# Optimization experiments

Hardware: AMD Instinct MI355X
Metric: run time of the kernel (lower is better)

Reference implementation:

```python
import jax, jax.numpy as jnp
import numpy as np

N_NODES = 100000
N_EDGES = 1600000
D_IN = 64
D_OUT = 64


def setup_inputs() -> dict:
    key = jax.random.key(0)
    k1, k2, k3, k4, k5 = jax.random.split(key, 5)
    features = jax.random.normal(k1, (N_NODES, D_IN), dtype=jnp.float32)
    edge_row = jax.random.randint(k2, (N_EDGES,), 0, N_NODES, dtype=jnp.int32)
    edge_col = jax.random.randint(k3, (N_EDGES,), 0, N_NODES, dtype=jnp.int32)
    edge_val = jax.random.uniform(k4, (N_EDGES,), dtype=jnp.float32)
    # learned parameters (xavier-uniform kernel, zero bias, ones skip weight)
    limit = float(np.sqrt(6.0 / (D_IN + D_OUT)))
    kernel = jax.random.uniform(k5, (D_IN, D_OUT), minval=-limit, maxval=limit, dtype=jnp.float32)
    bias = jnp.zeros((D_OUT,), dtype=jnp.float32)
    skip_weight = jnp.ones((D_OUT,), dtype=jnp.float32)
    return {
        "features": features,
        "kernel": kernel,
        "bias": bias,
        "skip_weight": skip_weight,
        "edge_row": edge_row,
        "edge_col": edge_col,
        "edge_val": edge_val,
    }


def reference(features, kernel, bias, skip_weight, edge_row, edge_col, edge_val):
    # dense projection: [n, d_in] @ [d_in, d_out]
    h = features @ kernel
    # SpMM: (A h)[r] = sum_{edges e with row r} val_e * h[col_e]
    gathered = h[edge_col] * edge_val[:, None]  # [n_edges, d_out]
    agg = jax.ops.segment_sum(gathered, edge_row, num_segments=N_NODES)
    out = h * skip_weight + agg + bias
    return jax.nn.selu(out)
```

## Files before the change

kernel.cpp:

```cpp
#include <hip/hip_runtime.h>
#include <math.h>

#define N_NODES 100000
#define N_EDGES 1600000
#define D 64
#define RPB 128
#define NBUK 782
#define CAP 3072
#define NGB 782
#define NHB 392
#define EPB 4096
#define POFF_STRIDE 392

typedef unsigned int u32;
typedef unsigned short u16;

static __device__ __forceinline__ u32 f2bf(float x) {
    u32 u = __float_as_uint(x);
    u32 r = u + 0x7FFFu + ((u >> 16) & 1u);
    return r >> 16;
}
static __device__ __forceinline__ u32 pack2(float a, float b) {
    return f2bf(a) | (f2bf(b) << 16);
}
static __device__ __forceinline__ float bflo(u32 u) { return __uint_as_float(u << 16); }
static __device__ __forceinline__ float bfhi(u32 u) { return __uint_as_float(u & 0xFFFF0000u); }
static __device__ __forceinline__ float selu(float x) {
    const float scale = 1.0507009873554805f;
    const float alpha = 1.6732632423543772f;
    return x > 0.f ? scale * x : scale * alpha * (expf(x) - 1.f);
}

__global__ __launch_bounds__(256) void fused_gemm_sort(
    const float* __restrict__ feat, const float* __restrict__ kern,
    const int* __restrict__ erow, const int* __restrict__ ecol,
    const float* __restrict__ eval, u16* __restrict__ hbf,
    int2* __restrict__ sedge, u32* __restrict__ poff)
{
    __shared__ u32 smem[4096];
    const int t = threadIdx.x;

    if (blockIdx.x >= NHB) {
        float* ks = (float*)smem;
        {
            const float4* k4 = (const float4*)kern;
            float4* ks4 = (float4*)ks;
            #pragma unroll
            for (int i = 0; i < 4; i++) ks4[t + 256 * i] = k4[t + 256 * i];
        }
        __syncthreads();

        const int cgi  = t & 7;
        const int rg   = t >> 3;
        const int row0 = (blockIdx.x - NHB) * RPB + rg * 4;

        float4 acc[4][2];
        #pragma unroll
        for (int r = 0; r < 4; r++)
            #pragma unroll
            for (int i = 0; i < 2; i++)
                acc[r][i] = make_float4(0.f, 0.f, 0.f, 0.f);

        #pragma unroll 4
        for (int s = 0; s < 16; s++) {
            float4 f[4];
            #pragma unroll
            for (int r = 0; r < 4; r++) {
                int row = min(row0 + r, N_NODES - 1);
                f[r] = ((const float4*)(feat + (size_t)row * D))[s];
            }
            float4 kk[4][2];
            #pragma unroll
            for (int kv = 0; kv < 4; kv++)
                #pragma unroll
                for (int i = 0; i < 2; i++)
                    kk[kv][i] = ((const float4*)(ks + (s * 4 + kv) * D))[cgi * 2 + i];
            #pragma unroll
            for (int r = 0; r < 4; r++) {
                #pragma unroll
                for (int kv = 0; kv < 4; kv++) {
                    float fv = (&f[r].x)[kv];
                    #pragma unroll
                    for (int i = 0; i < 2; i++) {
                        acc[r][i].x += fv * kk[kv][i].x;
                        acc[r][i].y += fv * kk[kv][i].y;
                        acc[r][i].z += fv * kk[kv][i].z;
                        acc[r][i].w += fv * kk[kv][i].w;
                    }
                }
            }
        }

        #pragma unroll
        for (int r = 0; r < 4; r++) {
            int row = row0 + r;
            if (row < N_NODES) {
                uint4 o;
                o.x = pack2(acc[r][0].x, acc[r][0].y);
                o.y = pack2(acc[r][0].z, acc[r][0].w);
                o.z = pack2(acc[r][1].x, acc[r][1].y);
                o.w = pack2(acc[r][1].z, acc[r][1].w);
                ((uint4*)(hbf + (size_t)row * D))[cgi] = o;
            }
        }
    } else {
        u32* c    = smem;
        u32* o    = c + NBUK;
        u32* cu   = o + NBUK + 1;
        u32* part = cu + NBUK;

        for (int i = t; i < NBUK; i += 256) c[i] = 0u;
        __syncthreads();

        const int hb   = blockIdx.x;
        const int base = hb * EPB;

        #pragma unroll
        for (int k = 0; k < 16; k++) {
            int i = base + k * 256 + t;
            if (i < N_EDGES) atomicAdd(&c[(u32)erow[i] >> 7], 1u);
        }
        __syncthreads();

        const int i0 = t * 4;
        {
            u32 p = 0u;
            #pragma unroll
            for (int j = 0; j < 4; j++) { int i = i0 + j; if (i < NBUK) p += c[i]; }
            part[t] = p;
        }
        __syncthreads();
        for (int d = 1; d < 256; d <<= 1) {
            u32 a = (t >= d) ? part[t - d] : 0u;
            __syncthreads();
            part[t] += a;
            __syncthreads();
        }
        {
            u32 run = (t > 0) ? part[t - 1] : 0u;
            #pragma unroll
            for (int j = 0; j < 4; j++) {
                int i = i0 + j;
                if (i < NBUK) { o[i] = run; cu[i] = run; run += c[i]; }
            }
            if (t == 255) o[NBUK] = part[255];
        }
        __syncthreads();

        #pragma unroll
        for (int k = 0; k < 16; k++) {
            int i = base + k * 256 + t;
            if (i < N_EDGES) {
                u32 r = (u32)erow[i];
                u32 rk = atomicAdd(&cu[r >> 7], 1u);
                sedge[(size_t)hb * EPB + rk] =
                    make_int2(ecol[i] | (int)((r & 127u) << 17),
                              __float_as_int(eval[i]));
            }
        }

        for (int i = t; i <= NBUK; i += 256)
            poff[(size_t)i * POFF_STRIDE + hb] = o[i];
    }
}

__global__ __launch_bounds__(1024) void agg_kernel(
    const u32* __restrict__ poff, const int2* __restrict__ sedge,
    const u16* __restrict__ hbf, const float* __restrict__ skip,
    const float* __restrict__ bias, float* __restrict__ out)
{
    __shared__ int2 eB[CAP];
    __shared__ u32 c[RPB];
    __shared__ u32 o[RPB];
    __shared__ u32 cur[RPB];
    __shared__ u32 rs0[NHB];
    __shared__ u32 rlen[NHB];

    const int t = threadIdx.x;
    const int w = t >> 6;
    const int lane = t & 63;
    const int b = blockIdx.x;

    if (t < RPB) c[t] = 0u;
    if (t < NHB) {
        u32 s0 = poff[(size_t)b * POFF_STRIDE + t];
        u32 s1 = poff[(size_t)(b + 1) * POFF_STRIDE + t];
        rs0[t]  = s0;
        rlen[t] = s1 - s0;
    }
    __syncthreads();

    for (int hb = w; hb < NHB; hb += 16) {
        u32 s0 = rs0[hb], len = rlen[hb];
        for (u32 j = (u32)lane; j < len; j += 64u) {
            int x = sedge[(size_t)hb * EPB + s0 + j].x;
            atomicAdd(&c[(u32)x >> 17], 1u);
        }
    }
    __syncthreads();

    if (t < RPB) o[t] = c[t];
    __syncthreads();
    for (int d = 1; d < RPB; d <<= 1) {
        u32 a = 0u;
        if (t < RPB && t >= d) a = o[t - d];
        __syncthreads();
        if (t < RPB) o[t] += a;
        __syncthreads();
    }
    if (t < RPB) { u32 e = o[t] - c[t]; o[t] = e; cur[t] = e; }
    __syncthreads();

    for (int hb = w; hb < NHB; hb += 16) {
        u32 s0 = rs0[hb], len = rlen[hb];
        for (u32 j = (u32)lane; j < len; j += 64u) {
            int2 e = sedge[(size_t)hb * EPB + s0 + j];
            u32 rl = (u32)e.x >> 17;
            u32 rk = atomicAdd(&cur[rl], 1u);
            if (rk < CAP) eB[rk] = make_int2(e.x & 0x1FFFF, e.y);
        }
    }
    __syncthreads();

    const int rows = min(RPB, N_NODES - b * RPB);
    const int g  = t >> 3;
    const int dg = t & 7;

    float a0 = 0.f, a1 = 0.f, a2 = 0.f, a3 = 0.f;
    float a4 = 0.f, a5 = 0.f, a6 = 0.f, a7 = 0.f;

    u32 jb = 0u, jend = 0u;
    if (g < rows) {
        jb = o[g];
        jend = min(jb + c[g], (u32)CAP);
    }

    u32 j = jb;
    for (; j + 3u < jend; j += 4u) {
        int2 e0 = eB[j];
        int2 e1 = eB[j + 1u];
        int2 e2 = eB[j + 2u];
        int2 e3 = eB[j + 3u];
        float v0 = __int_as_float(e0.y);
        float v1 = __int_as_float(e1.y);
        float v2 = __int_as_float(e2.y);
        float v3 = __int_as_float(e3.y);
        uint4 h0 = ((const uint4*)(hbf + (size_t)e0.x * D))[dg];
        uint4 h1 = ((const uint4*)(hbf + (size_t)e1.x * D))[dg];
        uint4 h2 = ((const uint4*)(hbf + (size_t)e2.x * D))[dg];
        uint4 h3 = ((const uint4*)(hbf + (size_t)e3.x * D))[dg];
        a0 += v0 * bflo(h0.x); a1 += v0 * bfhi(h0.x);
        a2 += v0 * bflo(h0.y); a3 += v0 * bfhi(h0.y);
        a4 += v0 * bflo(h0.z); a5 += v0 * bfhi(h0.z);
        a6 += v0 * bflo(h0.w); a7 += v0 * bfhi(h0.w);
        a0 += v1 * bflo(h1.x); a1 += v1 * bfhi(h1.x);
        a2 += v1 * bflo(h1.y); a3 += v1 * bfhi(h1.y);
        a4 += v1 * bflo(h1.z); a5 += v1 * bfhi(h1.z);
        a6 += v1 * bflo(h1.w); a7 += v1 * bfhi(h1.w);
        a0 += v2 * bflo(h2.x); a1 += v2 * bfhi(h2.x);
        a2 += v2 * bflo(h2.y); a3 += v2 * bfhi(h2.y);
        a4 += v2 * bflo(h2.z); a5 += v2 * bfhi(h2.z);
        a6 += v2 * bflo(h2.w); a7 += v2 * bfhi(h2.w);
        a0 += v3 * bflo(h3.x); a1 += v3 * bfhi(h3.x);
        a2 += v3 * bflo(h3.y); a3 += v3 * bfhi(h3.y);
        a4 += v3 * bflo(h3.z); a5 += v3 * bfhi(h3.z);
        a6 += v3 * bflo(h3.w); a7 += v3 * bfhi(h3.w);
    }
    for (; j < jend; j++) {
        int2 e0 = eB[j];
        float v0 = __int_as_float(e0.y);
        uint4 h0 = ((const uint4*)(hbf + (size_t)e0.x * D))[dg];
        a0 += v0 * bflo(h0.x); a1 += v0 * bfhi(h0.x);
        a2 += v0 * bflo(h0.y); a3 += v0 * bfhi(h0.y);
        a4 += v0 * bflo(h0.z); a5 += v0 * bfhi(h0.z);
        a6 += v0 * bflo(h0.w); a7 += v0 * bfhi(h0.w);
    }

    if (g < rows) {
        const int grow = b * RPB + g;
        uint4 hr = ((const uint4*)(hbf + (size_t)grow * D))[dg];
        float4 s0 = ((const float4*)skip)[2 * dg];
        float4 s1 = ((const float4*)skip)[2 * dg + 1];
        float4 b0 = ((const float4*)bias)[2 * dg];
        float4 b1 = ((const float4*)bias)[2 * dg + 1];
        float4 x0, x1;
        x0.x = selu(bflo(hr.x) * s0.x + b0.x + a0);
        x0.y = selu(bfhi(hr.x) * s0.y + b0.y + a1);
        x0.z = selu(bflo(hr.y) * s0.z + b0.z + a2);
        x0.w = selu(bfhi(hr.y) * s0.w + b0.w + a3);
        x1.x = selu(bflo(hr.z) * s1.x + b1.x + a4);
        x1.y = selu(bfhi(hr.z) * s1.y + b1.y + a5);
        x1.z = selu(bflo(hr.w) * s1.z + b1.z + a6);
        x1.w = selu(bfhi(hr.w) * s1.w + b1.w + a7);
        ((float4*)(out + (size_t)grow * D))[2 * dg]     = x0;
        ((float4*)(out + (size_t)grow * D))[2 * dg + 1] = x1;
    }
}

extern "C" void kernel_launch(void* const* d_in, const int* in_sizes, int n_in,
                              void* d_out, int out_size, void* d_ws, size_t ws_size,
                              hipStream_t stream)
{
    const float* feat = (const float*)d_in[0];
    const float* kern = (const float*)d_in[1];
    const float* bias = (const float*)d_in[2];
    const float* skip = (const float*)d_in[3];
    const int*   erow = (const int*)d_in[4];
    const int*   ecol = (const int*)d_in[5];
    const float* eval = (const float*)d_in[6];
    float* out = (float*)d_out;

    u16*  hbf   = (u16*)d_ws;
    u32*  poff  = (u32*)(hbf + (size_t)N_NODES * D);
    int2* sedge = (int2*)(poff + 306936);

    hipLaunchKernelGGL(fused_gemm_sort, dim3(NGB + NHB), dim3(256), 0, stream,
                       feat, kern, erow, ecol, eval, hbf, sedge, poff);
    hipLaunchKernelGGL(agg_kernel, dim3(NBUK), dim3(1024), 0, stream,
                       poff, sedge, hbf, skip, bias, out);
}
```

Before: 195.0 us.

## Flatten per-bucket edge gather with prefix scan and stage edges in LDS

The aggregation kernel used to walk the 392 bucket segments one wavefront at a time, with mostly idle lanes on short segments, and it read each edge from global memory twice. Now it prefix-scans the segment lengths, has all 1024 threads sweep a flattened edge index using a binary search to locate each segment, and caches the edges in a new LDS buffer eA. The second pass then reads from LDS instead of global memory. This costs extra LDS (another CAP int2 array), a 512-wide scan with several barriers, and a per-edge binary search. Edges beyond CAP are now dropped before counting rather than after the atomic rank.

```diff
diff --git a/kernel.cpp b/kernel.cpp
--- a/kernel.cpp
+++ b/kernel.cpp
@@ -169,33 +169,51 @@
     const u16* __restrict__ hbf, const float* __restrict__ skip,
     const float* __restrict__ bias, float* __restrict__ out)
 {
+    __shared__ int2 eA[CAP];
     __shared__ int2 eB[CAP];
     __shared__ u32 c[RPB];
     __shared__ u32 o[RPB];
     __shared__ u32 cur[RPB];
     __shared__ u32 rs0[NHB];
-    __shared__ u32 rlen[NHB];
+    __shared__ u32 rb[NHB + 1];
+    __shared__ u32 scn[512];
 
     const int t = threadIdx.x;
-    const int w = t >> 6;
-    const int lane = t & 63;
     const int b = blockIdx.x;
 
     if (t < RPB) c[t] = 0u;
+    u32 mylen = 0u;
     if (t < NHB) {
         u32 s0 = poff[(size_t)b * POFF_STRIDE + t];
         u32 s1 = poff[(size_t)(b + 1) * POFF_STRIDE + t];
-        rs0[t]  = s0;
-        rlen[t] = s1 - s0;
-    }
-    __syncthreads();
-
-    for (int hb = w; hb < NHB; hb += 16) {
-        u32 s0 = rs0[hb], len = rlen[hb];
-        for (u32 j = (u32)lane; j < len; j += 64u) {
-            int x = sedge[(size_t)hb * EPB + s0 + j].x;
-            atomicAdd(&c[(u32)x >> 17], 1u);
-        }
+        rs0[t] = s0;
+        mylen  = s1 - s0;
+    }
+    if (t < 512) scn[t] = (t < NHB) ? mylen : 0u;
+    __syncthreads();
+
+    for (int d = 1; d < 512; d <<= 1) {
+        u32 a = 0u;
+        if (t < 512 && t >= d) a = scn[t - d];
+        __syncthreads();
+        if (t < 512) scn[t] += a;
+        __syncthreads();
+    }
+    if (t == 0) rb[0] = 0u;
+    if (t < NHB) rb[t + 1] = scn[t];
+    __syncthreads();
+
+    const u32 cnt = min(rb[NHB], (u32)CAP);
+
+    for (u32 j = (u32)t; j < cnt; j += 1024u) {
+        u32 lo = 0u, hi = (u32)NHB;
+        while (hi - lo > 1u) {
+            u32 mid = (lo + hi) >> 1;
+            if (rb[mid] <= j) lo = mid; else hi = mid;
+        }
+        int2 e = sedge[(size_t)lo * EPB + rs0[lo] + (j - rb[lo])];
+        eA[j] = e;
+        atomicAdd(&c[(u32)e.x >> 17], 1u);
     }
     __syncthreads();
 
@@ -211,14 +229,11 @@
     if (t < RPB) { u32 e = o[t] - c[t]; o[t] = e; cur[t] = e; }
     __syncthreads();
 
-    for (int hb = w; hb < NHB; hb += 16) {
-        u32 s0 = rs0[hb], len = rlen[hb];
-        for (u32 j = (u32)lane; j < len; j += 64u) {
-            int2 e = sedge[(size_t)hb * EPB + s0 + j];
-            u32 rl = (u32)e.x >> 17;
-            u32 rk = atomicAdd(&cur[rl], 1u);
-            if (rk < CAP) eB[rk] = make_int2(e.x & 0x1FFFF, e.y);
-        }
+    for (u32 j = (u32)t; j < cnt; j += 1024u) {
+        int2 e = eA[j];
+        u32 rl = (u32)e.x >> 17;
+        u32 rk = atomicAdd(&cur[rl], 1u);
+        eB[rk] = make_int2(e.x & 0x1FFFF, e.y);
     }
     __syncthreads();
 
```

After: 173.7 us. 1.12x faster.
